# Optimization experiments

Measured on AMD Instinct MI355X. Metric: run time of the kernel, lower is better.

## Reference

```python
import jax, jax.numpy as jnp
import numpy as np
import math

B, N, D_MODEL, H, D_HEAD = 8, 1024, 1024, 16, 64
EPS = 1e-5

def layer_norm(x, g, b):
    mu = jnp.mean(x, axis=-1, keepdims=True)
    var = jnp.mean((x - mu) ** 2, axis=-1, keepdims=True)
    return (x - mu) * jax.lax.rsqrt(var + EPS) * g + b

def setup_inputs() -> dict:
    key = jax.random.key(0)
    ks = jax.random.split(key, 16)
    s = 1.0 / math.sqrt(D_MODEL)
    return {
        "queries": jax.random.normal(ks[0], (B, N, D_MODEL), jnp.float32),
        "keys": jax.random.normal(ks[1], (B, N, D_MODEL), jnp.float32),
        "values": jax.random.normal(ks[2], (B, N, D_MODEL), jnp.float32),
        "Wq": jax.random.uniform(ks[3], (H, D_MODEL, D_HEAD), jnp.float32, -s, s),
        "bq": jax.random.uniform(ks[4], (H, 1, D_HEAD), jnp.float32, -s, s),
        "Wk": jax.random.uniform(ks[5], (H, D_MODEL, D_HEAD), jnp.float32, -s, s),
        "bk": jax.random.uniform(ks[6], (H, 1, D_HEAD), jnp.float32, -s, s),
        "Wv": jax.random.uniform(ks[7], (H, D_MODEL, D_HEAD), jnp.float32, -s, s),
        "bv": jax.random.uniform(ks[8], (H, 1, D_HEAD), jnp.float32, -s, s),
        "W1": jax.random.uniform(ks[9], (D_MODEL, D_MODEL), jnp.float32, -s, s),
        "b1": jax.random.uniform(ks[10], (D_MODEL,), jnp.float32, -s, s),
        "W2": jax.random.uniform(ks[11], (D_MODEL, D_MODEL), jnp.float32, -s, s),
        "b2": jax.random.uniform(ks[12], (D_MODEL,), jnp.float32, -s, s),
        "g1": jnp.ones((D_MODEL,), jnp.float32),
        "be1": jnp.zeros((D_MODEL,), jnp.float32),
        "g2": jnp.ones((D_MODEL,), jnp.float32),
        "be2": jnp.zeros((D_MODEL,), jnp.float32),
    }

def reference(queries, keys, values, Wq, bq, Wk, bk, Wv, bv, W1, b1, W2, b2, g1, be1, g2, be2):
    # per-head projections: [B,H,N,Dh]
    q = jnp.einsum('bnd,hde->bhne', queries, Wq) + bq[None]
    k = jnp.einsum('bnd,hde->bhne', keys, Wk) + bk[None]
    v = jnp.einsum('bnd,hde->bhne', values, Wv) + bv[None]
    # custom scaling: sqrt(num_heads * d_head)
    scale = math.sqrt(H * D_HEAD)
    scores = jnp.einsum('bhqe,bhke->bhqk', q, k) / scale
    attn = jax.nn.softmax(scores, axis=-1)
    out = jnp.einsum('bhqk,bhke->bhqe', attn, v)  # [B,H,N,Dh]
    # interleaved head concat: transpose(1,2).transpose(2,3).reshape -> [B,N,Dh*H] with H fastest
    mha = jnp.transpose(out, (0, 2, 3, 1)).reshape(B, N, D_HEAD * H)
    mha = mha + queries  # residual
    h = layer_norm(mha, g1, be1)
    ffn = jnp.maximum(h @ W1 + b1, 0.0) @ W2 + b2
    h = h + ffn
    return layer_norm(h, g2, be2)
```

## Files before the change

### kernel.cpp

```cpp
#include <hip/hip_runtime.h>
#include <math.h>

#define D_MODEL 1024
#define NHEADS  16
#define DHEAD   64
#define BATCH   8
#define SEQ     1024
#define MROWS   (BATCH*SEQ)

typedef short          bf16x8 __attribute__((ext_vector_type(8)));
typedef unsigned short u16x8  __attribute__((ext_vector_type(8)));
typedef float          f32x4  __attribute__((ext_vector_type(4)));

typedef __attribute__((address_space(1))) void* gvp;
typedef __attribute__((address_space(3))) void* svp;

__device__ __forceinline__ unsigned short f2bf(float f) {
    unsigned int u = __float_as_uint(f);
    u = u + 0x7fffu + ((u >> 16) & 1u);
    return (unsigned short)(u >> 16);
}

__global__ __launch_bounds__(256) void convert3(
    const float* __restrict__ q, const float* __restrict__ k, const float* __restrict__ v,
    unsigned short* __restrict__ oq, unsigned short* __restrict__ ok, unsigned short* __restrict__ ov)
{
    const float* in; unsigned short* out;
    if (blockIdx.z == 0)      { in = q; out = oq; }
    else if (blockIdx.z == 1) { in = k; out = ok; }
    else                      { in = v; out = ov; }
    const size_t i = ((size_t)blockIdx.x * 256 + threadIdx.x) * 8;
    const float4 a = *(const float4*)(in + i);
    const float4 b = *(const float4*)(in + i + 4);
    u16x8 o;
    o[0] = f2bf(a.x); o[1] = f2bf(a.y); o[2] = f2bf(a.z); o[3] = f2bf(a.w);
    o[4] = f2bf(b.x); o[5] = f2bf(b.y); o[6] = f2bf(b.z); o[7] = f2bf(b.w);
    *(u16x8*)(out + i) = o;
}

__global__ __launch_bounds__(256) void tconvW(
    const float* __restrict__ Wq, const float* __restrict__ Wk, const float* __restrict__ Wv,
    const float* __restrict__ W1, const float* __restrict__ W2,
    unsigned short* __restrict__ Tq, unsigned short* __restrict__ Tk, unsigned short* __restrict__ Tv,
    unsigned short* __restrict__ T1, unsigned short* __restrict__ T2)
{
    const int z = blockIdx.z;
    const float* in; unsigned short* out;
    if (z == 0)      { in = Wq; out = Tq; }
    else if (z == 1) { in = Wk; out = Tk; }
    else if (z == 2) { in = Wv; out = Tv; }
    else if (z == 3) { in = W1; out = T1; }
    else             { in = W2; out = T2; }
    const int proj = (z < 3);

    __shared__ float t[32][33];
    const int c0 = blockIdx.x * 32, r0 = blockIdx.y * 32;
    const int tx = threadIdx.x & 31, ty = threadIdx.x >> 5;

    #pragma unroll
    for (int i = 0; i < 4; ++i) {
        const int r = r0 + ty + i * 8;
        const size_t addr = proj
            ? ((size_t)(c0 >> 6) * (D_MODEL * DHEAD) + (size_t)r * DHEAD + (c0 & 63) + tx)
            : ((size_t)r * D_MODEL + c0 + tx);
        t[ty + i * 8][tx] = in[addr];
    }
    __syncthreads();
    #pragma unroll
    for (int i = 0; i < 4; ++i) {
        const int n = c0 + ty + i * 8;
        out[(size_t)n * D_MODEL + r0 + tx] = f2bf(t[tx][ty + i * 8]);
    }
}

template<int EPI>
__global__ __launch_bounds__(256) void gemm128(
    const unsigned short* __restrict__ A,
    const unsigned short* __restrict__ Bt,
    const float* __restrict__ bias,
    const float* __restrict__ res,
    void* __restrict__ outp)
{
    const int m0 = blockIdx.x * 128;
    const int n0 = blockIdx.y * 128;
    const int tid = threadIdx.x;
    const int l  = tid & 63;
    const int w  = tid >> 6;
    const int wr = w >> 1, wc = w & 1;
    const int lr = l & 15, lk = l >> 4;

    __shared__ unsigned short As[128 * 32];
    __shared__ unsigned short Bs[128 * 32];

    f32x4 acc[4][4] = {};

    const int r_a = (l >> 2);
    const int c_a = (l & 3) * 8;

    for (int k0 = 0; k0 < D_MODEL; k0 += 32) {
        #pragma unroll
        for (int i = 0; i < 2; ++i) {
            const int c   = w * 2 + i;
            const int row = c * 16 + r_a;
            __builtin_amdgcn_global_load_lds(
                (gvp)(void*)&A [(size_t)(m0 + row) * D_MODEL + k0 + c_a],
                (svp)(void*)&As[c * 512], 16, 0, 0);
            __builtin_amdgcn_global_load_lds(
                (gvp)(void*)&Bt[(size_t)(n0 + row) * D_MODEL + k0 + c_a],
                (svp)(void*)&Bs[c * 512], 16, 0, 0);
        }
        __syncthreads();

        bf16x8 af[4], bf[4];
        #pragma unroll
        for (int m = 0; m < 4; ++m)
            af[m] = *(const bf16x8*)&As[(wr * 64 + m * 16 + lr) * 32 + lk * 8];
        #pragma unroll
        for (int n = 0; n < 4; ++n)
            bf[n] = *(const bf16x8*)&Bs[(wc * 64 + n * 16 + lr) * 32 + lk * 8];
        #pragma unroll
        for (int m = 0; m < 4; ++m)
            #pragma unroll
            for (int n = 0; n < 4; ++n)
                acc[m][n] = __builtin_amdgcn_mfma_f32_16x16x32_bf16(af[m], bf[n], acc[m][n], 0, 0, 0);
        __syncthreads();
    }

    const int col_base = n0 + wc * 64;
    const int row_base = m0 + wr * 64;
    #pragma unroll
    for (int n = 0; n < 4; ++n) {
        const int col  = col_base + n * 16 + lr;
        const float bc = bias[col];
        #pragma unroll
        for (int m = 0; m < 4; ++m) {
            if (EPI == 1) {
                const int row0 = row_base + m * 16 + lk * 4;
                const int b = row0 >> 10, nn0 = row0 & 1023;
                ushort4 pk;
                pk.x = f2bf(acc[m][n][0] + bc);
                pk.y = f2bf(acc[m][n][1] + bc);
                pk.z = f2bf(acc[m][n][2] + bc);
                pk.w = f2bf(acc[m][n][3] + bc);
                *(ushort4*)&((unsigned short*)outp)[((size_t)b * 1024 + col) * SEQ + nn0] = pk;
            } else {
                #pragma unroll
                for (int r = 0; r < 4; ++r) {
                    const int row = row_base + m * 16 + lk * 4 + r;
                    const float v = acc[m][n][r] + bc;
                    if (EPI == 0)
                        ((unsigned short*)outp)[(size_t)row * D_MODEL + col] = f2bf(v);
                    if (EPI == 2)
                        ((unsigned short*)outp)[(size_t)row * D_MODEL + col] = f2bf(fmaxf(v, 0.f));
                    if (EPI == 3)
                        ((float*)outp)[(size_t)row * D_MODEL + col] = v + res[(size_t)row * D_MODEL + col];
                }
            }
        }
    }
}

__global__ __launch_bounds__(256) void attn_mfma(
    const unsigned short* __restrict__ q16,
    const unsigned short* __restrict__ k16,
    const unsigned short* __restrict__ vt,
    float* __restrict__ omha)
{
    const int qt = blockIdx.x;
    const int h  = blockIdx.y;
    const int b  = blockIdx.z;
    const int tid = threadIdx.x;
    const int l  = tid & 63, w = tid >> 6;
    const int lr = l & 15, lk = l >> 4;

    __shared__ unsigned short Ks[64 * 72];
    __shared__ unsigned short Vs[64 * 72];
    __shared__ unsigned short Ps[4][16 * 72];

    const size_t qrow = ((size_t)b * SEQ + qt * 64 + w * 16 + lr) * D_MODEL + h * DHEAD;
    const bf16x8 qf0 = *(const bf16x8*)&q16[qrow + lk * 8];
    const bf16x8 qf1 = *(const bf16x8*)&q16[qrow + 32 + lk * 8];

    f32x4 O[4] = {};
    float mrow[4] = {-1e30f, -1e30f, -1e30f, -1e30f};
    float lrow[4] = {0.f, 0.f, 0.f, 0.f};

    const int str = tid >> 3;
    const int stc = (tid & 7) * 8;
    const size_t kbase = (size_t)b * SEQ * D_MODEL + h * DHEAD;
    const size_t vbase = ((size_t)b * 1024 + h * DHEAD) * SEQ;

    for (int kt = 0; kt < SEQ / 64; ++kt) {
        __syncthreads();
        *(u16x8*)&Ks[str * 72 + stc]        = *(const u16x8*)&k16[kbase + (size_t)(kt * 64 + str) * D_MODEL + stc];
        *(u16x8*)&Ks[(str + 32) * 72 + stc] = *(const u16x8*)&k16[kbase + (size_t)(kt * 64 + str + 32) * D_MODEL + stc];
        *(u16x8*)&Vs[str * 72 + stc]        = *(const u16x8*)&vt [vbase + (size_t)str * SEQ + kt * 64 + stc];
        *(u16x8*)&Vs[(str + 32) * 72 + stc] = *(const u16x8*)&vt [vbase + (size_t)(str + 32) * SEQ + kt * 64 + stc];
        __syncthreads();

        f32x4 sf[4];
        #pragma unroll
        for (int f = 0; f < 4; ++f) {
            const bf16x8 kf0 = *(const bf16x8*)&Ks[(f * 16 + lr) * 72 + lk * 8];
            const bf16x8 kf1 = *(const bf16x8*)&Ks[(f * 16 + lr) * 72 + 32 + lk * 8];
            f32x4 s = {};
            s = __builtin_amdgcn_mfma_f32_16x16x32_bf16(qf0, kf0, s, 0, 0, 0);
            s = __builtin_amdgcn_mfma_f32_16x16x32_bf16(qf1, kf1, s, 0, 0, 0);
            s *= 0.03125f;
            sf[f] = s;
        }

        float alpha[4];
        #pragma unroll
        for (int r = 0; r < 4; ++r) {
            float mx = fmaxf(fmaxf(sf[0][r], sf[1][r]), fmaxf(sf[2][r], sf[3][r]));
            mx = fmaxf(mx, __shfl_xor(mx, 1));
            mx = fmaxf(mx, __shfl_xor(mx, 2));
            mx = fmaxf(mx, __shfl_xor(mx, 4));
            mx = fmaxf(mx, __shfl_xor(mx, 8));
            const float mnew = fmaxf(mrow[r], mx);
            alpha[r] = __expf(mrow[r] - mnew);
            mrow[r] = mnew;
        }
        float psum[4] = {0.f, 0.f, 0.f, 0.f};
        #pragma unroll
        for (int f = 0; f < 4; ++f)
            #pragma unroll
            for (int r = 0; r < 4; ++r) {
                const float p = __expf(sf[f][r] - mrow[r]);
                psum[r] += p;
                Ps[w][(lk * 4 + r) * 72 + f * 16 + lr] = f2bf(p);
            }
        #pragma unroll
        for (int r = 0; r < 4; ++r) {
            float ps = psum[r];
            ps += __shfl_xor(ps, 1);
            ps += __shfl_xor(ps, 2);
            ps += __shfl_xor(ps, 4);
            ps += __shfl_xor(ps, 8);
            lrow[r] = lrow[r] * alpha[r] + ps;
        }
        #pragma unroll
        for (int f = 0; f < 4; ++f)
            #pragma unroll
            for (int r = 0; r < 4; ++r)
                O[f][r] *= alpha[r];

        const bf16x8 pa0 = *(const bf16x8*)&Ps[w][lr * 72 + lk * 8];
        const bf16x8 pa1 = *(const bf16x8*)&Ps[w][lr * 72 + 32 + lk * 8];
        #pragma unroll
        for (int f = 0; f < 4; ++f) {
            const bf16x8 vf0 = *(const bf16x8*)&Vs[(f * 16 + lr) * 72 + lk * 8];
            const bf16x8 vf1 = *(const bf16x8*)&Vs[(f * 16 + lr) * 72 + 32 + lk * 8];
            O[f] = __builtin_amdgcn_mfma_f32_16x16x32_bf16(pa0, vf0, O[f], 0, 0, 0);
            O[f] = __builtin_amdgcn_mfma_f32_16x16x32_bf16(pa1, vf1, O[f], 0, 0, 0);
        }
    }

    #pragma unroll
    for (int f = 0; f < 4; ++f)
        #pragma unroll
        for (int r = 0; r < 4; ++r) {
            const float ov = O[f][r] / lrow[r];
            omha[((size_t)b * SEQ + qt * 64 + w * 16 + lk * 4 + r) * D_MODEL + h * DHEAD + f * 16 + lr] = ov;
        }
}

__global__ __launch_bounds__(256) void ln1_kernel(
    const float* __restrict__ mha, const float* __restrict__ qres,
    const float* __restrict__ g, const float* __restrict__ be,
    float* __restrict__ hf, unsigned short* __restrict__ h16)
{
    const int row = blockIdx.x, tid = threadIdx.x;
    const size_t base = (size_t)row * D_MODEL;
    __shared__ float buf[D_MODEL];

    *(float4*)&buf[tid * 4] = *(const float4*)&mha[base + tid * 4];
    __syncthreads();

    const float4 qv = *(const float4*)&qres[base + tid * 4];
    const float qa[4] = {qv.x, qv.y, qv.z, qv.w};
    float x[4], s = 0.f, sq = 0.f;
    #pragma unroll
    for (int j = 0; j < 4; ++j) {
        const int c = tid * 4 + j;
        x[j] = buf[(c & 15) * 64 + (c >> 4)] + qa[j];
        s += x[j]; sq += x[j] * x[j];
    }
    #pragma unroll
    for (int off = 32; off >= 1; off >>= 1) {
        s  += __shfl_down(s,  off);
        sq += __shfl_down(sq, off);
    }
    __shared__ float sa[4], sb[4];
    if ((tid & 63) == 0) { sa[tid >> 6] = s; sb[tid >> 6] = sq; }
    __syncthreads();
    const float tot = sa[0] + sa[1] + sa[2] + sa[3];
    const float tsq = sb[0] + sb[1] + sb[2] + sb[3];
    const float mean = tot * (1.f / D_MODEL);
    const float var  = tsq * (1.f / D_MODEL) - mean * mean;
    const float rstd = rsqrtf(var + 1e-5f);

    const float4 gv = *(const float4*)&g[tid * 4];
    const float4 bv = *(const float4*)&be[tid * 4];
    const float ga[4] = {gv.x, gv.y, gv.z, gv.w};
    const float ba[4] = {bv.x, bv.y, bv.z, bv.w};
    float y[4];
    #pragma unroll
    for (int j = 0; j < 4; ++j) y[j] = (x[j] - mean) * rstd * ga[j] + ba[j];
    float4 of; of.x = y[0]; of.y = y[1]; of.z = y[2]; of.w = y[3];
    *(float4*)&hf[base + tid * 4] = of;
    unsigned short h4[4];
    #pragma unroll
    for (int j = 0; j < 4; ++j) h4[j] = f2bf(y[j]);
    *(uint2*)&h16[base + tid * 4] = *(uint2*)h4;
}

__global__ __launch_bounds__(256) void ln2_kernel(
    const float* __restrict__ xin,
    const float* __restrict__ g, const float* __restrict__ be,
    float* __restrict__ out)
{
    const int row = blockIdx.x, tid = threadIdx.x;
    const size_t base = (size_t)row * D_MODEL;
    float4 xv = *(const float4*)&xin[base + tid * 4];
    float s  = xv.x + xv.y + xv.z + xv.w;
    float sq = xv.x*xv.x + xv.y*xv.y + xv.z*xv.z + xv.w*xv.w;
    #pragma unroll
    for (int off = 32; off >= 1; off >>= 1) {
        s  += __shfl_down(s,  off);
        sq += __shfl_down(sq, off);
    }
    __shared__ float sa[4], sb[4];
    if ((tid & 63) == 0) { sa[tid >> 6] = s; sb[tid >> 6] = sq; }
    __syncthreads();
    const float tot = sa[0] + sa[1] + sa[2] + sa[3];
    const float tsq = sb[0] + sb[1] + sb[2] + sb[3];
    const float mean = tot * (1.f / D_MODEL);
    const float var  = tsq * (1.f / D_MODEL) - mean * mean;
    const float rstd = rsqrtf(var + 1e-5f);
    const float4 gv = *(const float4*)&g[tid * 4];
    const float4 bv = *(const float4*)&be[tid * 4];
    float4 ov;
    ov.x = (xv.x - mean) * rstd * gv.x + bv.x;
    ov.y = (xv.y - mean) * rstd * gv.y + bv.y;
    ov.z = (xv.z - mean) * rstd * gv.z + bv.z;
    ov.w = (xv.w - mean) * rstd * gv.w + bv.w;
    *(float4*)&out[base + tid * 4] = ov;
}

extern "C" void kernel_launch(void* const* d_in, const int* in_sizes, int n_in,
                              void* d_out, int out_size, void* d_ws, size_t ws_size,
                              hipStream_t stream)
{
    (void)in_sizes; (void)n_in; (void)out_size; (void)ws_size;
    const float* queries = (const float*)d_in[0];
    const float* keys    = (const float*)d_in[1];
    const float* values  = (const float*)d_in[2];
    const float* Wq = (const float*)d_in[3];
    const float* bq = (const float*)d_in[4];
    const float* Wk = (const float*)d_in[5];
    const float* bk = (const float*)d_in[6];
    const float* Wv = (const float*)d_in[7];
    const float* bv = (const float*)d_in[8];
    const float* W1 = (const float*)d_in[9];
    const float* b1 = (const float*)d_in[10];
    const float* W2 = (const float*)d_in[11];
    const float* b2 = (const float*)d_in[12];
    const float* g1 = (const float*)d_in[13];
    const float* be1= (const float*)d_in[14];
    const float* g2 = (const float*)d_in[15];
    const float* be2= (const float*)d_in[16];
    float* out = (float*)d_out;

    const size_t SZ16 = (size_t)MROWS * D_MODEL * 2;
    const size_t SZW  = (size_t)D_MODEL * D_MODEL * 2;
    char* p = (char*)d_ws;
    unsigned short* XQ  = (unsigned short*)(p);
    unsigned short* XK  = (unsigned short*)(p + SZ16);
    unsigned short* XV  = (unsigned short*)(p + 2 * SZ16);
    unsigned short* TWq = (unsigned short*)(p + 3 * SZ16);
    unsigned short* TWk = (unsigned short*)(p + 3 * SZ16 + SZW);
    unsigned short* TWv = (unsigned short*)(p + 3 * SZ16 + 2 * SZW);
    unsigned short* TW1 = (unsigned short*)(p + 3 * SZ16 + 3 * SZW);
    unsigned short* TW2 = (unsigned short*)(p + 3 * SZ16 + 4 * SZW);
    char* p2 = p + 3 * SZ16 + 5 * SZW;
    unsigned short* Q16 = (unsigned short*)(p2);
    unsigned short* K16 = (unsigned short*)(p2 + SZ16);
    unsigned short* VT  = (unsigned short*)(p2 + 2 * SZ16);
    float*          MHA = (float*)XQ;
    float*          HF  = (float*)Q16;
    unsigned short* H16 = VT;
    unsigned short* F1  = XV;
    float*          Y   = MHA;

    const dim3 blk(256);

    convert3<<<dim3(MROWS * D_MODEL / (256 * 8), 1, 3), blk, 0, stream>>>(
        queries, keys, values, XQ, XK, XV);
    tconvW<<<dim3(32, 32, 5), blk, 0, stream>>>(
        Wq, Wk, Wv, W1, W2, TWq, TWk, TWv, TW1, TW2);

    const dim3 gg(MROWS / 128, D_MODEL / 128);
    gemm128<0><<<gg, blk, 0, stream>>>(XQ, TWq, bq, nullptr, Q16);
    gemm128<0><<<gg, blk, 0, stream>>>(XK, TWk, bk, nullptr, K16);
    gemm128<1><<<gg, blk, 0, stream>>>(XV, TWv, bv, nullptr, VT);

    attn_mfma<<<dim3(SEQ / 64, NHEADS, BATCH), blk, 0, stream>>>(Q16, K16, VT, MHA);

    ln1_kernel<<<dim3(MROWS), blk, 0, stream>>>(MHA, queries, g1, be1, HF, H16);

    gemm128<2><<<gg, blk, 0, stream>>>(H16, TW1, b1, nullptr, F1);
    gemm128<3><<<gg, blk, 0, stream>>>(F1,  TW2, b2, HF, Y);

    ln2_kernel<<<dim3(MROWS), blk, 0, stream>>>(Y, g2, be2, out);
}
```

Before: 461.8 us.

## Merge QKV projections into one launch and restructure attention softmax layout

The three Q/K/V projection GEMMs become a single launch over grid z, and the 1/32 score scale is folded into the Q projection epilogue. The attention kernel computes S transposed so each lane holds a full query row's scores. That reduces the max/sum reductions to two cross-lane shuffles, and P is written to LDS with packed bf16 converts. It also skips the O rescale when no row max changed, adds s_setprio around the MFMA sections, and uses reciprocal multiplies in the output. The aim is to cut launch overhead and softmax ALU/shuffle work, at the cost of more complex lane-to-row mapping.

```diff
diff --git a/kernel.cpp b/kernel.cpp
--- a/kernel.cpp
+++ b/kernel.cpp
@@ -73,14 +73,21 @@
     }
 }
 
-template<int EPI>
-__global__ __launch_bounds__(256) void gemm128(
-    const unsigned short* __restrict__ A,
-    const unsigned short* __restrict__ Bt,
-    const float* __restrict__ bias,
-    const float* __restrict__ res,
-    void* __restrict__ outp)
-{
+__global__ __launch_bounds__(256) void proj3_gemm(
+    const unsigned short* __restrict__ XQ, const unsigned short* __restrict__ XK,
+    const unsigned short* __restrict__ XV,
+    const unsigned short* __restrict__ TWq, const unsigned short* __restrict__ TWk,
+    const unsigned short* __restrict__ TWv,
+    const float* __restrict__ bq, const float* __restrict__ bk, const float* __restrict__ bv,
+    unsigned short* __restrict__ Q16, unsigned short* __restrict__ K16,
+    unsigned short* __restrict__ VT)
+{
+    const int z = blockIdx.z;
+    const unsigned short* A  = (z == 0) ? XQ  : (z == 1) ? XK  : XV;
+    const unsigned short* Bt = (z == 0) ? TWq : (z == 1) ? TWk : TWv;
+    const float* bias        = (z == 0) ? bq  : (z == 1) ? bk  : bv;
+    const float oscale       = (z == 0) ? 0.03125f : 1.0f;
+
     const int m0 = blockIdx.x * 128;
     const int n0 = blockIdx.y * 128;
     const int tid = threadIdx.x;
@@ -134,7 +141,7 @@
         const float bc = bias[col];
         #pragma unroll
         for (int m = 0; m < 4; ++m) {
-            if (EPI == 1) {
+            if (z == 2) {
                 const int row0 = row_base + m * 16 + lk * 4;
                 const int b = row0 >> 10, nn0 = row0 & 1023;
                 ushort4 pk;
@@ -142,19 +149,88 @@
                 pk.y = f2bf(acc[m][n][1] + bc);
                 pk.z = f2bf(acc[m][n][2] + bc);
                 pk.w = f2bf(acc[m][n][3] + bc);
-                *(ushort4*)&((unsigned short*)outp)[((size_t)b * 1024 + col) * SEQ + nn0] = pk;
+                *(ushort4*)&VT[((size_t)b * 1024 + col) * SEQ + nn0] = pk;
             } else {
+                unsigned short* outp = (z == 0) ? Q16 : K16;
                 #pragma unroll
                 for (int r = 0; r < 4; ++r) {
                     const int row = row_base + m * 16 + lk * 4 + r;
-                    const float v = acc[m][n][r] + bc;
-                    if (EPI == 0)
-                        ((unsigned short*)outp)[(size_t)row * D_MODEL + col] = f2bf(v);
-                    if (EPI == 2)
-                        ((unsigned short*)outp)[(size_t)row * D_MODEL + col] = f2bf(fmaxf(v, 0.f));
-                    if (EPI == 3)
-                        ((float*)outp)[(size_t)row * D_MODEL + col] = v + res[(size_t)row * D_MODEL + col];
+                    outp[(size_t)row * D_MODEL + col] = f2bf((acc[m][n][r] + bc) * oscale);
                 }
+            }
+        }
+    }
+}
+
+template<int EPI>
+__global__ __launch_bounds__(256) void gemm128(
+    const unsigned short* __restrict__ A,
+    const unsigned short* __restrict__ Bt,
+    const float* __restrict__ bias,
+    const float* __restrict__ res,
+    void* __restrict__ outp)
+{
+    const int m0 = blockIdx.x * 128;
+    const int n0 = blockIdx.y * 128;
+    const int tid = threadIdx.x;
+    const int l  = tid & 63;
+    const int w  = tid >> 6;
+    const int wr = w >> 1, wc = w & 1;
+    const int lr = l & 15, lk = l >> 4;
+
+    __shared__ unsigned short As[128 * 32];
+    __shared__ unsigned short Bs[128 * 32];
+
+    f32x4 acc[4][4] = {};
+
+    const int r_a = (l >> 2);
+    const int c_a = (l & 3) * 8;
+
+    for (int k0 = 0; k0 < D_MODEL; k0 += 32) {
+        #pragma unroll
+        for (int i = 0; i < 2; ++i) {
+            const int c   = w * 2 + i;
+            const int row = c * 16 + r_a;
+            __builtin_amdgcn_global_load_lds(
+                (gvp)(void*)&A [(size_t)(m0 + row) * D_MODEL + k0 + c_a],
+                (svp)(void*)&As[c * 512], 16, 0, 0);
+            __builtin_amdgcn_global_load_lds(
+                (gvp)(void*)&Bt[(size_t)(n0 + row) * D_MODEL + k0 + c_a],
+                (svp)(void*)&Bs[c * 512], 16, 0, 0);
+        }
+        __syncthreads();
+
+        bf16x8 af[4], bf[4];
+        #pragma unroll
+        for (int m = 0; m < 4; ++m)
+            af[m] = *(const bf16x8*)&As[(wr * 64 + m * 16 + lr) * 32 + lk * 8];
+        #pragma unroll
+        for (int n = 0; n < 4; ++n)
+            bf[n] = *(const bf16x8*)&Bs[(wc * 64 + n * 16 + lr) * 32 + lk * 8];
+        #pragma unroll
+        for (int m = 0; m < 4; ++m)
+            #pragma unroll
+            for (int n = 0; n < 4; ++n)
+                acc[m][n] = __builtin_amdgcn_mfma_f32_16x16x32_bf16(af[m], bf[n], acc[m][n], 0, 0, 0);
+        __syncthreads();
+    }
+
+    const int col_base = n0 + wc * 64;
+    const int row_base = m0 + wr * 64;
+    #pragma unroll
+    for (int n = 0; n < 4; ++n) {
+        const int col  = col_base + n * 16 + lr;
+        const float bc = bias[col];
+        #pragma unroll
+        for (int m = 0; m < 4; ++m) {
+            #pragma unroll
+            for (int r = 0; r < 4; ++r) {
+                const int row = row_base + m * 16 + lk * 4 + r;
+                float v = acc[m][n][r] + bc;
+                if (EPI == 2)
+                    ((unsigned short*)outp)[(size_t)row * D_MODEL + col] = f2bf(fmaxf(v, 0.f));
+                if (EPI == 3)
+                    ((float*)outp)[(size_t)row * D_MODEL + col] = v + res[(size_t)row * D_MODEL + col];
             }
         }
     }
@@ -182,8 +258,8 @@
     const bf16x8 qf1 = *(const bf16x8*)&q16[qrow + 32 + lk * 8];
 
     f32x4 O[4] = {};
-    float mrow[4] = {-1e30f, -1e30f, -1e30f, -1e30f};
-    float lrow[4] = {0.f, 0.f, 0.f, 0.f};
+    float m_l = -1e30f;
+    float l_l = 0.f;
 
     const int str = tid >> 3;
     const int stc = (tid & 7) * 8;
@@ -198,56 +274,66 @@
         *(u16x8*)&Vs[(str + 32) * 72 + stc] = *(const u16x8*)&vt [vbase + (size_t)(str + 32) * SEQ + kt * 64 + stc];
         __syncthreads();
 
-        f32x4 sf[4];
+        f32x4 st[4];
+        __builtin_amdgcn_s_setprio(1);
         #pragma unroll
         for (int f = 0; f < 4; ++f) {
             const bf16x8 kf0 = *(const bf16x8*)&Ks[(f * 16 + lr) * 72 + lk * 8];
             const bf16x8 kf1 = *(const bf16x8*)&Ks[(f * 16 + lr) * 72 + 32 + lk * 8];
             f32x4 s = {};
-            s = __builtin_amdgcn_mfma_f32_16x16x32_bf16(qf0, kf0, s, 0, 0, 0);
-            s = __builtin_amdgcn_mfma_f32_16x16x32_bf16(qf1, kf1, s, 0, 0, 0);
-            s *= 0.03125f;
-            sf[f] = s;
-        }
-
-        float alpha[4];
-        #pragma unroll
-        for (int r = 0; r < 4; ++r) {
-            float mx = fmaxf(fmaxf(sf[0][r], sf[1][r]), fmaxf(sf[2][r], sf[3][r]));
-            mx = fmaxf(mx, __shfl_xor(mx, 1));
-            mx = fmaxf(mx, __shfl_xor(mx, 2));
-            mx = fmaxf(mx, __shfl_xor(mx, 4));
-            mx = fmaxf(mx, __shfl_xor(mx, 8));
-            const float mnew = fmaxf(mrow[r], mx);
-            alpha[r] = __expf(mrow[r] - mnew);
-            mrow[r] = mnew;
-        }
-        float psum[4] = {0.f, 0.f, 0.f, 0.f};
+            s = __builtin_amdgcn_mfma_f32_16x16x32_bf16(kf0, qf0, s, 0, 0, 0);
+            s = __builtin_amdgcn_mfma_f32_16x16x32_bf16(kf1, qf1, s, 0, 0, 0);
+            st[f] = s;
+        }
+        __builtin_amdgcn_s_setprio(0);
+
+        float mx = st[0][0];
+        #pragma unroll
+        for (int f = 0; f < 4; ++f)
+            #pragma unroll
+            for (int r = 0; r < 4; ++r) mx = fmaxf(mx, st[f][r]);
+        mx = fmaxf(mx, __shfl_xor(mx, 16));
+        mx = fmaxf(mx, __shfl_xor(mx, 32));
+        const float mnew = fmaxf(m_l, mx);
+        const float alpha = __expf(m_l - mnew);
+        m_l = mnew;
+
+        float psum = 0.f;
         #pragma unroll
         for (int f = 0; f < 4; ++f)
             #pragma unroll
             for (int r = 0; r < 4; ++r) {
-                const float p = __expf(sf[f][r] - mrow[r]);
-                psum[r] += p;
-                Ps[w][(lk * 4 + r) * 72 + f * 16 + lr] = f2bf(p);
+                const float pv = __expf(st[f][r] - mnew);
+                st[f][r] = pv;
+                psum += pv;
             }
-        #pragma unroll
-        for (int r = 0; r < 4; ++r) {
-            float ps = psum[r];
-            ps += __shfl_xor(ps, 1);
-            ps += __shfl_xor(ps, 2);
-            ps += __shfl_xor(ps, 4);
-            ps += __shfl_xor(ps, 8);
-            lrow[r] = lrow[r] * alpha[r] + ps;
-        }
-        #pragma unroll
-        for (int f = 0; f < 4; ++f)
+        psum += __shfl_xor(psum, 16);
+        psum += __shfl_xor(psum, 32);
+        l_l = l_l * alpha + psum;
+
+        #pragma unroll
+        for (int f = 0; f < 4; ++f) {
+            unsigned int plo, phi;
+            asm("v_cvt_pk_bf16_f32 %0, %1, %2" : "=v"(plo) : "v"(st[f][0]), "v"(st[f][1]));
+            asm("v_cvt_pk_bf16_f32 %0, %1, %2" : "=v"(phi) : "v"(st[f][2]), "v"(st[f][3]));
+            uint2 pk; pk.x = plo; pk.y = phi;
+            *(uint2*)&Ps[w][lr * 72 + f * 16 + lk * 4] = pk;
+        }
+
+        if (!__all(alpha == 1.0f)) {
+            const float a0 = __shfl(alpha, lk * 4 + 0);
+            const float a1 = __shfl(alpha, lk * 4 + 1);
+            const float a2 = __shfl(alpha, lk * 4 + 2);
+            const float a3 = __shfl(alpha, lk * 4 + 3);
             #pragma unroll
-            for (int r = 0; r < 4; ++r)
-                O[f][r] *= alpha[r];
+            for (int f = 0; f < 4; ++f) {
+                O[f][0] *= a0; O[f][1] *= a1; O[f][2] *= a2; O[f][3] *= a3;
+            }
+        }
 
         const bf16x8 pa0 = *(const bf16x8*)&Ps[w][lr * 72 + lk * 8];
         const bf16x8 pa1 = *(const bf16x8*)&Ps[w][lr * 72 + 32 + lk * 8];
+        __builtin_amdgcn_s_setprio(1);
         #pragma unroll
         for (int f = 0; f < 4; ++f) {
             const bf16x8 vf0 = *(const bf16x8*)&Vs[(f * 16 + lr) * 72 + lk * 8];
@@ -255,15 +341,21 @@
             O[f] = __builtin_amdgcn_mfma_f32_16x16x32_bf16(pa0, vf0, O[f], 0, 0, 0);
             O[f] = __builtin_amdgcn_mfma_f32_16x16x32_bf16(pa1, vf1, O[f], 0, 0, 0);
         }
-    }
-
-    #pragma unroll
-    for (int f = 0; f < 4; ++f)
-        #pragma unroll
-        for (int r = 0; r < 4; ++r) {
-            const float ov = O[f][r] / lrow[r];
-            omha[((size_t)b * SEQ + qt * 64 + w * 16 + lk * 4 + r) * D_MODEL + h * DHEAD + f * 16 + lr] = ov;
-        }
+        __builtin_amdgcn_s_setprio(0);
+    }
+
+    const float il0 = 1.f / __shfl(l_l, lk * 4 + 0);
+    const float il1 = 1.f / __shfl(l_l, lk * 4 + 1);
+    const float il2 = 1.f / __shfl(l_l, lk * 4 + 2);
+    const float il3 = 1.f / __shfl(l_l, lk * 4 + 3);
+    #pragma unroll
+    for (int f = 0; f < 4; ++f) {
+        const size_t obase = ((size_t)b * SEQ + qt * 64 + w * 16 + lk * 4) * D_MODEL + h * DHEAD + f * 16 + lr;
+        omha[obase]               = O[f][0] * il0;
+        omha[obase + D_MODEL]     = O[f][1] * il1;
+        omha[obase + 2 * D_MODEL] = O[f][2] * il2;
+        omha[obase + 3 * D_MODEL] = O[f][3] * il3;
+    }
 }
 
 __global__ __launch_bounds__(256) void ln1_kernel(
@@ -401,15 +493,14 @@
     tconvW<<<dim3(32, 32, 5), blk, 0, stream>>>(
         Wq, Wk, Wv, W1, W2, TWq, TWk, TWv, TW1, TW2);
 
+    proj3_gemm<<<dim3(MROWS / 128, D_MODEL / 128, 3), blk, 0, stream>>>(
+        XQ, XK, XV, TWq, TWk, TWv, bq, bk, bv, Q16, K16, VT);
+
+    attn_mfma<<<dim3(SEQ / 64, NHEADS, BATCH), blk, 0, stream>>>(Q16, K16, VT, MHA);
+
+    ln1_kernel<<<dim3(MROWS), blk, 0, stream>>>(MHA, queries, g1, be1, HF, H16);
+
     const dim3 gg(MROWS / 128, D_MODEL / 128);
-    gemm128<0><<<gg, blk, 0, stream>>>(XQ, TWq, bq, nullptr, Q16);
-    gemm128<0><<<gg, blk, 0, stream>>>(XK, TWk, bk, nullptr, K16);
-    gemm128<1><<<gg, blk, 0, stream>>>(XV, TWv, bv, nullptr, VT);
-
-    attn_mfma<<<dim3(SEQ / 64, NHEADS, BATCH), blk, 0, stream>>>(Q16, K16, VT, MHA);
-
-    ln1_kernel<<<dim3(MROWS), blk, 0, stream>>>(MHA, queries, g1, be1, HF, H16);
-
     gemm128<2><<<gg, blk, 0, stream>>>(H16, TW1, b1, nullptr, F1);
     gemm128<3><<<gg, blk, 0, stream>>>(F1,  TW2, b2, HF, Y);
 
```

After: 409.6 us. 1.13x faster.
